# Kernel optimization log

Hardware: AMD Instinct MI355X
Metric: run time of the kernel (lower is better)

Reference implementation:

```python
import jax, jax.numpy as jnp
import numpy as np

B, T, PAST, HID = 2, 512, 4096, 4096
HQ, HKV, D = 32, 8, 128
HH_SIZE, RECENT = 512, 512
CACHE = HH_SIZE + RECENT
MAX_POS = PAST + T


def rotate_half(x):
    h = x.shape[-1] // 2
    return jnp.concatenate([-x[..., h:], x[..., :h]], axis=-1)


def setup_inputs() -> dict:
    key = jax.random.key(0)
    ks = jax.random.split(key, 9)
    hidden_states = jax.random.normal(ks[0], (B, T, HID), jnp.float32) * 0.02
    past_k = jax.random.normal(ks[1], (B, HKV, PAST, D), jnp.float32)
    past_v = jax.random.normal(ks[2], (B, HKV, PAST, D), jnp.float32)
    # accumulated heavy-hitter scores are nonnegative attention-mass sums
    hh_prev = jax.random.uniform(ks[3], (B, HKV, PAST), jnp.float32) * float(T)
    wq = jax.random.normal(ks[4], (HID, HQ * D), jnp.float32) * 0.02
    wk = jax.random.normal(ks[5], (HID, HKV * D), jnp.float32) * 0.02
    wv = jax.random.normal(ks[6], (HID, HKV * D), jnp.float32) * 0.02
    wo = jax.random.normal(ks[7], (HQ * D, HID), jnp.float32) * 0.02
    # RoPE tables [1, MAX_POS, D]
    inv_freq = 1.0 / (10000.0 ** (jnp.arange(0, D, 2, dtype=jnp.float32) / D))
    t = jnp.arange(MAX_POS, dtype=jnp.float32)
    freqs = jnp.einsum('t,f->tf', t, inv_freq)
    emb = jnp.concatenate([freqs, freqs], axis=-1)
    cos = jnp.cos(emb)[None]
    sin = jnp.sin(emb)[None]
    position_ids = jnp.broadcast_to(PAST + jnp.arange(T, dtype=jnp.int32)[None, :], (B, T))
    return {"hidden_states": hidden_states, "past_k": past_k, "past_v": past_v,
            "hh_prev": hh_prev, "wq": wq, "wk": wk, "wv": wv, "wo": wo,
            "cos": cos, "sin": sin, "position_ids": position_ids}


def reference(hidden_states, past_k, past_v, hh_prev, wq, wk, wv, wo, cos, sin, position_ids):
    b, t, _ = hidden_states.shape
    # projections -> [B, H, T, D]
    q = (hidden_states @ wq).reshape(b, t, HQ, D).transpose(0, 2, 1, 3)
    k_new = (hidden_states @ wk).reshape(b, t, HKV, D).transpose(0, 2, 1, 3)
    v_new = (hidden_states @ wv).reshape(b, t, HKV, D).transpose(0, 2, 1, 3)
    # RoPE: gather cos/sin at position_ids -> [B, 1, T, D]
    cos_g = cos[0][position_ids][:, None]
    sin_g = sin[0][position_ids][:, None]
    q = q * cos_g + rotate_half(q) * sin_g
    k_new = k_new * cos_g + rotate_half(k_new) * sin_g
    k = jnp.concatenate([past_k, k_new], axis=2)   # [B, HKV, S, D]
    v = jnp.concatenate([past_v, v_new], axis=2)
    s = k.shape[2]
    past_len = s - t
    g = HQ // HKV
    k_rep = jnp.repeat(k, g, axis=1)               # repeat_interleave over heads
    v_rep = jnp.repeat(v, g, axis=1)
    scores = jnp.einsum('bhtd,bhsd->bhts', q, k_rep) / jnp.sqrt(jnp.float32(D))
    causal = jnp.arange(s)[None, :] <= (past_len + jnp.arange(t))[:, None]  # [T, S]
    scores = jnp.where(causal[None, None], scores, jnp.finfo(scores.dtype).min)
    attn = jax.nn.softmax(scores, axis=-1)         # [B, HQ, T, S]
    ctx = jnp.einsum('bhts,bhsd->bhtd', attn, v_rep)
    out = ctx.transpose(0, 2, 1, 3).reshape(b, t, HQ * D) @ wo
    # --- H2O heavy-hitter score update ('average' GQA reduction) ---
    sc = attn.sum(axis=2)                          # [B, HQ, S]
    sc = sc.reshape(b, HKV, g, s).mean(axis=2)     # [B, HKV, S]
    hh = sc.at[:, :, :past_len].add(hh_prev)
    # --- eviction: topk heavy hitters outside recent window + recent window ---
    select = hh[:, :, : s - RECENT]
    _, top = jax.lax.top_k(select, HH_SIZE)
    top = jnp.sort(top, axis=-1)
    recent_idx = jnp.broadcast_to(jnp.arange(s - RECENT, s, dtype=top.dtype), (b, HKV, RECENT))
    keep = jnp.concatenate([top, recent_idx], axis=-1)      # [B, HKV, CACHE]
    k_kept = jnp.take_along_axis(k, keep[..., None], axis=2)
    v_kept = jnp.take_along_axis(v, keep[..., None], axis=2)
    hh_new = jnp.take_along_axis(hh, keep, axis=2)
    return out, k_kept, v_kept, hh_new
```

## Files before the change

### kernel.cpp

```cpp
#include <hip/hip_runtime.h>
#include <cstdint>
#include <cstddef>

typedef unsigned short u16;
typedef __attribute__((ext_vector_type(8))) short short8;
typedef __attribute__((ext_vector_type(4))) float floatx4;

static __device__ __forceinline__ u16 f2bf(float f){
  union { float f; uint32_t i; } u; u.f = f;
  uint32_t i = u.i;
  return (u16)((i + 0x7FFFu + ((i >> 16) & 1u)) >> 16);
}

struct __align__(8) U16x4 { u16 a,b,c,d; };

__global__ void k_convert(const float* __restrict__ src, u16* __restrict__ dst, int n4){
  int i = blockIdx.x*256 + threadIdx.x;
  if (i >= n4) return;
  float4 v = ((const float4*)src)[i];
  U16x4 o{f2bf(v.x), f2bf(v.y), f2bf(v.z), f2bf(v.w)};
  ((U16x4*)dst)[i] = o;
}

__global__ void k_copy_pastk(const float* __restrict__ pk, u16* __restrict__ kcat){
  int i = blockIdx.x*256 + threadIdx.x;
  int slice = i >> 17;
  int off   = i & 131071;
  float4 v = ((const float4*)pk)[i];
  U16x4 o{f2bf(v.x), f2bf(v.y), f2bf(v.z), f2bf(v.w)};
  ((U16x4*)(kcat + (size_t)slice*(4608*128)))[off] = o;
}

__global__ void k_transpose(const float* __restrict__ src, u16* __restrict__ dst,
                            int lds_, int ldd, size_t sstride, size_t dstride){
  src += (size_t)blockIdx.z * sstride; dst += (size_t)blockIdx.z * dstride;
  __shared__ float tile[32][33];
  int bm = blockIdx.y*32, bn = blockIdx.x*32;
  int tx = threadIdx.x & 31, ty = threadIdx.x >> 5;
  #pragma unroll
  for (int r = 0; r < 32; r += 8)
    tile[r+ty][tx] = src[(size_t)(bm + r + ty)*lds_ + bn + tx];
  __syncthreads();
  #pragma unroll
  for (int r = 0; r < 32; r += 8)
    dst[(size_t)(bn + r + ty)*ldd + bm + tx] = f2bf(tile[tx][r+ty]);
}

__global__ __launch_bounds__(256) void k_gemm_bt(
    const u16* __restrict__ A, const u16* __restrict__ Bt, float* __restrict__ C,
    int N, int Kfull, int kLen, size_t cstride)
{
  __shared__ __align__(16) u16 As[128*64];
  __shared__ __align__(16) u16 Bs[128*64];
  const int tid = threadIdx.x, lane = tid & 63, wave = tid >> 6;
  const int m0 = blockIdx.y*128, n0 = blockIdx.x*128;
  const int kOff = blockIdx.z * kLen;
  C += (size_t)blockIdx.z * cstride;
  const int wr = (wave >> 1)*64, wc = (wave & 1)*64;
  const int srow = tid >> 3, sc8 = tid & 7;
  const u16* ap = A  + (size_t)(m0 + srow)*Kfull + kOff + sc8*8;
  const u16* bp = Bt + (size_t)(n0 + srow)*Kfull + kOff + sc8*8;
  floatx4 acc[4][4] = {};
  short8 ra[4], rb[4];
  #pragma unroll
  for (int i = 0; i < 4; ++i){
    ra[i] = *(const short8*)(ap + (size_t)i*32*Kfull);
    rb[i] = *(const short8*)(bp + (size_t)i*32*Kfull);
  }
  const int nk = kLen >> 6;
  for (int kt = 0; kt < nk; ++kt){
    #pragma unroll
    for (int i = 0; i < 4; ++i){
      const int r = srow + i*32;
      const int c = sc8 ^ (r & 7);
      *(short8*)(As + r*64 + c*8) = ra[i];
      *(short8*)(Bs + r*64 + c*8) = rb[i];
    }
    __syncthreads();
    if (kt + 1 < nk){
      const size_t ko = (size_t)(kt+1)*64;
      #pragma unroll
      for (int i = 0; i < 4; ++i){
        ra[i] = *(const short8*)(ap + (size_t)i*32*Kfull + ko);
        rb[i] = *(const short8*)(bp + (size_t)i*32*Kfull + ko);
      }
    }
    #pragma unroll
    for (int ks = 0; ks < 2; ++ks){
      const int c16 = ks*4 + (lane >> 4);
      short8 af[4], bf[4];
      #pragma unroll
      for (int mi = 0; mi < 4; ++mi){
        const int r = wr + mi*16 + (lane & 15);
        af[mi] = *(const short8*)(As + r*64 + ((c16 ^ (r & 7))*8));
      }
      #pragma unroll
      for (int ni = 0; ni < 4; ++ni){
        const int r = wc + ni*16 + (lane & 15);
        bf[ni] = *(const short8*)(Bs + r*64 + ((c16 ^ (r & 7))*8));
      }
      #pragma unroll
      for (int mi = 0; mi < 4; ++mi)
        #pragma unroll
        for (int ni = 0; ni < 4; ++ni)
          acc[mi][ni] = __builtin_amdgcn_mfma_f32_16x16x32_bf16(af[mi], bf[ni], acc[mi][ni], 0,0,0);
    }
    __syncthreads();
  }
  #pragma unroll
  for (int mi = 0; mi < 4; ++mi)
    #pragma unroll
    for (int ni = 0; ni < 4; ++ni){
      const int col = n0 + wc + ni*16 + (lane & 15);
      const int row = m0 + wr + mi*16 + ((lane >> 4) << 2);
      #pragma unroll
      for (int j = 0; j < 4; ++j)
        C[(size_t)(row + j)*N + col] = acc[mi][ni][j];
    }
}

__global__ void k_add(const float* __restrict__ a, const float* __restrict__ b,
                      float* __restrict__ o, int n4){
  int i = blockIdx.x*256 + threadIdx.x;
  if (i >= n4) return;
  float4 x = ((const float4*)a)[i], y = ((const float4*)b)[i];
  float4 z; z.x=x.x+y.x; z.y=x.y+y.y; z.z=x.z+y.z; z.w=x.w+y.w;
  ((float4*)o)[i] = z;
}

__global__ void k_rope_q(const float* __restrict__ qfA, const float* __restrict__ qfB,
                         const float* __restrict__ cosb, const float* __restrict__ sinb,
                         const int* __restrict__ pid, u16* __restrict__ qbo){
  int gid = blockIdx.x*256 + threadIdx.x;
  int d = gid & 63, hh = (gid >> 6) & 31, m = gid >> 11;
  int b = m >> 9, t = m & 511;
  int p = pid[b*512 + t];
  float c = cosb[(size_t)p*128 + d], s = sinb[(size_t)p*128 + d];
  size_t ib = (size_t)m*4096 + hh*128 + d;
  float x = qfA[ib] + qfB[ib], y = qfA[ib+64] + qfB[ib+64];
  const float sc = 0.08838834764831845f;
  size_t ob = (((size_t)(b*32 + hh))*512 + t)*128 + d;
  qbo[ob]      = f2bf((x*c - y*s)*sc);
  qbo[ob + 64] = f2bf((y*c + x*s)*sc);
}

__global__ void k_rope_kv(const float* __restrict__ kvfA, const float* __restrict__ kvfB,
                          const float* __restrict__ cosb, const float* __restrict__ sinb,
                          const int* __restrict__ pid,
                          u16* __restrict__ kcat, u16* __restrict__ vtcat){
  int gid = blockIdx.x*256 + threadIdx.x;
  int d = gid & 63, kv = (gid >> 6) & 7, m = gid >> 9;
  int b = m >> 9, t = m & 511;
  int p = pid[b*512 + t];
  float c = cosb[(size_t)p*128 + d], s = sinb[(size_t)p*128 + d];
  size_t ib = (size_t)m*2048 + kv*128 + d;
  float x = kvfA[ib] + kvfB[ib], y = kvfA[ib+64] + kvfB[ib+64];
  float k0 = x*c - y*s, k1 = y*c + x*s;
  int bk = b*8 + kv;
  size_t kb = ((size_t)bk*4608 + 4096 + t)*128 + d;
  kcat[kb] = f2bf(k0); kcat[kb + 64] = f2bf(k1);
  float v0 = kvfA[ib+1024] + kvfB[ib+1024];
  float v1 = kvfA[ib+1088] + kvfB[ib+1088];
  size_t vb = (size_t)bk*(128*4608) + (size_t)d*4608 + 4096 + t;
  vtcat[vb] = f2bf(v0);
  vtcat[vb + (size_t)64*4608] = f2bf(v1);
}

__global__ __launch_bounds__(256) void k_attn_l(
    const u16* __restrict__ qb, const u16* __restrict__ kcat,
    float* __restrict__ lpart)
{
  __shared__ __align__(16) u16 kl[64*128];
  const int tid = threadIdx.x, lane = tid & 63, wave = tid >> 6;
  const int bid = blockIdx.x;
  const int slice = (bid & 7) + 8*(bid >> 10);
  const int within = (bid >> 3) & 127;
  const int b = slice >> 3, kv = slice & 7;
  const int h = kv*4 + (within >> 5);
  const int tb = (within >> 2) & 7;
  const int sc = within & 3;
  const int t0 = tb*64;
  const int ntiles = 65 + tb;
  const int st0 = sc*18;
  const int st1 = (st0 + 18 < ntiles) ? (st0 + 18) : ntiles;
  const u16* qp = qb + (((size_t)(b*32+h))*512 + t0)*128;
  const u16* kp = kcat + (size_t)slice*(4608*128);

  short8 qf[4];
  {
    const int r = wave*16 + (lane & 15);
    const u16* q0 = qp + (size_t)r*128 + ((lane>>4)*8);
    #pragma unroll
    for (int ks=0; ks<4; ++ks) qf[ks] = *(const short8*)(q0 + ks*32);
  }
  const int c16 = tid & 15, srow = tid >> 4;
  short8 rk[4];
  #pragma unroll
  for (int i=0;i<4;++i)
    rk[i] = *(const short8*)(kp + (size_t)(st0*64 + i*16 + srow)*128 + c16*8);

  float l0=0.f,l1=0.f,l2=0.f,l3=0.f;
  for (int st=st0; st<st1; ++st){
    __syncthreads();
    #pragma unroll
    for (int i=0;i<4;++i){
      const int row = i*16 + srow;
      *(short8*)(kl + row*128 + ((c16 ^ (row&7))*8)) = rk[i];
    }
    __syncthreads();
    if (st+1 < st1){
      #pragma unroll
      for (int i=0;i<4;++i)
        rk[i] = *(const short8*)(kp + (size_t)((st+1)*64 + i*16 + srow)*128 + c16*8);
    }
    floatx4 sacc[4] = {};
    #pragma unroll
    for (int ks=0; ks<4; ++ks){
      const int cc = ks*4 + (lane>>4);
      #pragma unroll
      for (int nf=0; nf<4; ++nf){
        const int r = nf*16 + (lane&15);
        short8 kf = *(const short8*)(kl + r*128 + ((cc ^ (r&7))*8));
        sacc[nf] = __builtin_amdgcn_mfma_f32_16x16x32_bf16(qf[ks], kf, sacc[nf], 0,0,0);
      }
    }
    const bool lastt = (st == ntiles-1);
    #pragma unroll
    for (int nf=0;nf<4;++nf)
      #pragma unroll
      for (int j=0;j<4;++j){
        float e = __expf(sacc[nf][j]);
        if (lastt){
          int scol = nf*16 + (lane&15);
          int tloc = wave*16 + ((lane>>4)<<2) + j;
          if (scol > tloc) e = 0.f;
        }
        if(j==0)l0+=e; else if(j==1)l1+=e; else if(j==2)l2+=e; else l3+=e;
      }
  }
  #pragma unroll
  for (int m=1; m<=8; m<<=1){
    l0 += __shfl_xor(l0,m); l1 += __shfl_xor(l1,m);
    l2 += __shfl_xor(l2,m); l3 += __shfl_xor(l3,m);
  }
  if ((lane & 15) == 0){
    float* lp = lpart + ((((size_t)(b*32+h))*8 + tb)<<8) + (sc<<6) + wave*16 + ((lane>>4)<<2);
    lp[0]=l0; lp[1]=l1; lp[2]=l2; lp[3]=l3;
  }
}

__global__ __launch_bounds__(256) void k_attn_pv(
    const u16* __restrict__ qb, const u16* __restrict__ kcat,
    const u16* __restrict__ vtcat, const float* __restrict__ lpart,
    u16* __restrict__ ctxb, float* __restrict__ part)
{
  __shared__ __align__(16) u16 kl[64*128];
  __shared__ __align__(16) u16 vl[128*64];
  __shared__ __align__(16) float plds[64*68];
  __shared__ float cw[4*64];

  const int tid=threadIdx.x, lane=tid&63, wave=tid>>6;
  const int bid=blockIdx.x;
  const int slice = (bid&7) + 8*((bid>>3)>>5);
  const int within = (bid>>3)&31;
  const int b=slice>>3, kv=slice&7;
  const int h = kv*4 + (within>>3);
  const int tb = within&7;
  const int t0 = tb*64;
  const int ntiles = 65+tb;
  const u16* qp = qb + (((size_t)(b*32+h))*512 + t0)*128;
  const u16* kp = kcat + (size_t)slice*(4608*128);
  const u16* vp = vtcat + (size_t)slice*(128*4608);
  float* pb = part + (((size_t)(b*32+h))*8 + tb)*4608;

  float rl[4];
  {
    const float* lp = lpart + ((((size_t)(b*32+h))*8 + tb)<<8);
    const int r0 = wave*16 + ((lane>>4)<<2);
    #pragma unroll
    for (int j=0;j<4;++j){
      int r = r0 + j;
      float l = lp[r] + lp[64+r] + lp[128+r] + lp[192+r];
      rl[j] = 1.f/l;
    }
  }
  short8 qf[4];
  {
    const int r = wave*16 + (lane & 15);
    const u16* q0 = qp + (size_t)r*128 + ((lane>>4)*8);
    #pragma unroll
    for (int ks=0; ks<4; ++ks) qf[ks] = *(const short8*)(q0 + ks*32);
  }
  const int c16 = tid&15, srow = tid>>4;
  const int vc = tid&7,  vrow = tid>>3;
  short8 rk[4], rv[4];
  #pragma unroll
  for (int i=0;i<4;++i){
    rk[i] = *(const short8*)(kp + (size_t)(i*16 + srow)*128 + c16*8);
    rv[i] = *(const short8*)(vp + (size_t)(i*32 + vrow)*4608 + vc*8);
  }
  floatx4 pacc[8] = {};
  const int prow = wave*16 + (lane&15);

  for (int st=0; st<ntiles; ++st){
    const int s0 = st*64;
    __syncthreads();
    if (st > 0 && tid < 64)
      pb[s0-64+tid] = cw[tid] + cw[64+tid] + cw[128+tid] + cw[192+tid];
    #pragma unroll
    for (int i=0;i<4;++i){
      const int row = i*16 + srow;
      *(short8*)(kl + row*128 + ((c16 ^ (row&7))*8)) = rk[i];
      const int vr = i*32 + vrow;
      *(short8*)(vl + vr*64 + ((vc ^ (vr&7))*8)) = rv[i];
    }
    __syncthreads();
    if (st+1 < ntiles){
      #pragma unroll
      for (int i=0;i<4;++i){
        rk[i] = *(const short8*)(kp + (size_t)((st+1)*64 + i*16 + srow)*128 + c16*8);
        rv[i] = *(const short8*)(vp + (size_t)(i*32 + vrow)*4608 + (st+1)*64 + vc*8);
      }
    }
    floatx4 sacc[4] = {};
    #pragma unroll
    for (int ks=0; ks<4; ++ks){
      const int cc = ks*4 + (lane>>4);
      #pragma unroll
      for (int nf=0; nf<4; ++nf){
        const int r = nf*16 + (lane&15);
        short8 kf = *(const short8*)(kl + r*128 + ((cc ^ (r&7))*8));
        sacc[nf] = __builtin_amdgcn_mfma_f32_16x16x32_bf16(qf[ks], kf, sacc[nf], 0,0,0);
      }
    }
    const bool lastt = (st==ntiles-1);
    float cs0=0.f, cs1=0.f, cs2=0.f, cs3=0.f;
    #pragma unroll
    for (int nf=0;nf<4;++nf){
      float cpart=0.f;
      #pragma unroll
      for (int j=0;j<4;++j){
        float e = __expf(sacc[nf][j]);
        if (lastt){
          int scol = nf*16 + (lane&15);
          int tloc = wave*16 + ((lane>>4)<<2) + j;
          if (scol > tloc) e = 0.f;
        }
        float p = e * rl[j];
        plds[(wave*16 + ((lane>>4)<<2) + j)*68 + nf*16 + (lane&15)] = p;
        cpart += p;
      }
      if(nf==0)cs0=cpart; else if(nf==1)cs1=cpart; else if(nf==2)cs2=cpart; else cs3=cpart;
    }
    cs0 += __shfl_xor(cs0,16); cs0 += __shfl_xor(cs0,32);
    cs1 += __shfl_xor(cs1,16); cs1 += __shfl_xor(cs1,32);
    cs2 += __shfl_xor(cs2,16); cs2 += __shfl_xor(cs2,32);
    cs3 += __shfl_xor(cs3,16); cs3 += __shfl_xor(cs3,32);
    {
      const int nfsel = lane >> 4;
      float v = (nfsel==0)?cs0:(nfsel==1)?cs1:(nfsel==2)?cs2:cs3;
      cw[wave*64 + nfsel*16 + (lane & 15)] = v;
    }
    short8 pa[2];
    #pragma unroll
    for (int k2 = 0; k2 < 2; ++k2){
      const int sbase = k2*32 + ((lane>>4)*8);
      const float* pp = plds + prow*68 + sbase;
      float4 x = *(const float4*)pp;
      float4 y = *(const float4*)(pp + 4);
      short8 t8;
      t8[0]=(short)f2bf(x.x); t8[1]=(short)f2bf(x.y); t8[2]=(short)f2bf(x.z); t8[3]=(short)f2bf(x.w);
      t8[4]=(short)f2bf(y.x); t8[5]=(short)f2bf(y.y); t8[6]=(short)f2bf(y.z); t8[7]=(short)f2bf(y.w);
      pa[k2] = t8;
    }
    #pragma unroll
    for (int nf = 0; nf < 8; ++nf){
      const int rv2 = nf*16 + (lane & 15);
      #pragma unroll
      for (int k2 = 0; k2 < 2; ++k2){
        const int c = ((k2*4 + (lane>>4)) ^ (rv2 & 7));
        short8 vf = *(const short8*)(vl + rv2*64 + c*8);
        pacc[nf] = __builtin_amdgcn_mfma_f32_16x16x32_bf16(pa[k2], vf, pacc[nf], 0,0,0);
      }
    }
  }
  __syncthreads();
  if (tid < 64)
    pb[(ntiles-1)*64 + tid] = cw[tid] + cw[64+tid] + cw[128+tid] + cw[192+tid];
  #pragma unroll
  for (int nf = 0; nf < 8; ++nf)
    #pragma unroll
    for (int j = 0; j < 4; ++j){
      const int trow = t0 + wave*16 + ((lane>>4)<<2) + j;
      const int col  = h*128 + nf*16 + (lane & 15);
      ctxb[(size_t)(b*512 + trow)*4096 + col] = f2bf(pacc[nf][j]);
    }
}

__global__ void k_hh_reduce(const float* __restrict__ part, const float* __restrict__ hhprev,
                            float* __restrict__ hh){
  int gid = blockIdx.x*256 + threadIdx.x;
  if (gid >= 73728) return;
  int s = gid % 4608; int bk = gid / 4608; int b = bk >> 3, kv = bk & 7;
  float acc = 0.f;
  #pragma unroll
  for (int h4 = 0; h4 < 4; ++h4){
    const float* pp = part + (((size_t)(b*32 + kv*4 + h4))*8)*4608 + s;
    #pragma unroll
    for (int tbb = 0; tbb < 8; ++tbb)
      if (s < 4160 + tbb*64) acc += pp[(size_t)tbb*4608];
  }
  acc *= 0.25f;
  if (s < 4096) acc += hhprev[(size_t)bk*4096 + s];
  hh[gid] = acc;
}

__global__ __launch_bounds__(256) void k_topk(const float* __restrict__ hh, int* __restrict__ keep,
                                              float* __restrict__ hh_new){
  __shared__ uint64_t keys[4096];
  __shared__ int sidx[512];
  const int bk = blockIdx.x, tid = threadIdx.x;
  const float* hp = hh + (size_t)bk*4608;
  for (int i = tid; i < 4096; i += 256){
    uint32_t vb = __float_as_uint(hp[i]);
    keys[i] = ((uint64_t)(0xFFFFFFFFu - vb) << 12) | (uint32_t)i;
  }
  __syncthreads();
  for (int k = 2; k <= 4096; k <<= 1){
    for (int j = k >> 1; j > 0; j >>= 1){
      for (int i = tid; i < 4096; i += 256){
        int ixj = i ^ j;
        if (ixj > i){
          uint64_t a = keys[i], c = keys[ixj];
          bool up = ((i & k) == 0);
          if ((a > c) == up){ keys[i] = c; keys[ixj] = a; }
        }
      }
      __syncthreads();
    }
  }
  for (int i = tid; i < 512; i += 256) sidx[i] = (int)(keys[i] & 0xFFF);
  __syncthreads();
  for (int k = 2; k <= 512; k <<= 1){
    for (int j = k >> 1; j > 0; j >>= 1){
      for (int i = tid; i < 512; i += 256){
        int ixj = i ^ j;
        if (ixj > i){
          int a = sidx[i], c = sidx[ixj];
          bool up = ((i & k) == 0);
          if ((a > c) == up){ sidx[i] = c; sidx[ixj] = a; }
        }
      }
      __syncthreads();
    }
  }
  for (int i = tid; i < 512; i += 256){
    int id = sidx[i];
    keep[bk*1024 + i] = id;
    hh_new[(size_t)bk*1024 + i] = hp[id];
    keep[bk*1024 + 512 + i] = 4096 + i;
    hh_new[(size_t)bk*1024 + 512 + i] = hp[4096 + i];
  }
}

__global__ void k_gather(const float* __restrict__ pastk, const float* __restrict__ pastv,
                         const float* __restrict__ kvfA, const float* __restrict__ kvfB,
                         const float* __restrict__ cosb, const float* __restrict__ sinb,
                         const int* __restrict__ pid, const int* __restrict__ keep,
                         float* __restrict__ outk, float* __restrict__ outv){
  int r = blockIdx.x*2 + (threadIdx.x >> 7);
  int d = threadIdx.x & 127;
  int bk = r >> 10, i = r & 1023;
  int idx = keep[bk*1024 + i];
  float kval, vval;
  if (idx < 4096){
    kval = pastk[((size_t)bk*4096 + idx)*128 + d];
    vval = pastv[((size_t)bk*4096 + idx)*128 + d];
  } else {
    int t = idx - 4096; int b = bk >> 3, kv = bk & 7;
    size_t base = ((size_t)(b*512 + t))*2048 + kv*128;
    int dp = (d < 64) ? d + 64 : d - 64;
    float x  = kvfA[base + d]  + kvfB[base + d];
    float xp = kvfA[base + dp] + kvfB[base + dp];
    int p = pid[b*512 + t];
    float c = cosb[(size_t)p*128 + d], s = sinb[(size_t)p*128 + d];
    kval = x*c + xp*((d < 64) ? -s : s);
    vval = kvfA[base + 1024 + d] + kvfB[base + 1024 + d];
  }
  outk[(size_t)r*128 + d] = kval;
  outv[(size_t)r*128 + d] = vval;
}

extern "C" void kernel_launch(void* const* d_in, const int* in_sizes, int n_in,
                              void* d_out, int out_size, void* d_ws, size_t ws_size,
                              hipStream_t stream){
  const float* hs     = (const float*)d_in[0];
  const float* pastk  = (const float*)d_in[1];
  const float* pastv  = (const float*)d_in[2];
  const float* hhprev = (const float*)d_in[3];
  const float* wq     = (const float*)d_in[4];
  const float* wk     = (const float*)d_in[5];
  const float* wv     = (const float*)d_in[6];
  const float* wo     = (const float*)d_in[7];
  const float* cosb   = (const float*)d_in[8];
  const float* sinb   = (const float*)d_in[9];
  const int*   pid    = (const int*)d_in[10];
  float* out = (float*)d_out;
  char* ws = (char*)d_ws;

  u16*   hsb  = (u16*)(ws + 0);
  u16*   wqt  = (u16*)(ws + 8388608);
  u16*   wkvt = (u16*)(ws + 41943040);
  float* qfA  = (float*)(ws + 58720256);
  float* qfB  = (float*)(ws + 75497472);
  float* kvfA = (float*)(ws + 92274688);
  float* kvfB = (float*)(ws + 100663296);
  u16*   qb   = (u16*)(ws + 109051904);
  u16*   kcat = (u16*)(ws + 117440512);
  u16*   vtc  = (u16*)(ws + 136314880);
  u16*   ctxb = (u16*)(ws + 155189248);
  float* part = (float*)(ws + 163577856);
  float* lprt = (float*)(ws + 173015040);
  float* hhb  = (float*)(ws + 173539328);
  int*   keep = (int*)(ws + 173834240);

  (void)in_sizes; (void)n_in; (void)out_size; (void)ws_size;

  k_convert<<<4096,256,0,stream>>>(hs, hsb, 1048576);
  k_transpose<<<dim3(128,128,1),256,0,stream>>>(wq, wqt, 4096, 4096, 0, 0);
  k_transpose<<<dim3(32,128,1),256,0,stream>>>(wk, wkvt, 1024, 4096, 0, 0);
  k_transpose<<<dim3(32,128,1),256,0,stream>>>(wv, wkvt + (size_t)1024*4096, 1024, 4096, 0, 0);
  k_transpose<<<dim3(4,128,16),256,0,stream>>>(pastv, vtc, 128, 4608,
                                               (size_t)4096*128, (size_t)128*4608);
  k_copy_pastk<<<8192,256,0,stream>>>(pastk, kcat);

  k_gemm_bt<<<dim3(32,8,2),256,0,stream>>>(hsb, wqt, qfA, 4096, 4096, 2048, (size_t)1024*4096);
  k_gemm_bt<<<dim3(16,8,2),256,0,stream>>>(hsb, wkvt, kvfA, 2048, 4096, 2048, (size_t)1024*2048);
  k_transpose<<<dim3(128,128,1),256,0,stream>>>(wo, wqt, 4096, 4096, 0, 0);

  k_rope_q<<<8192,256,0,stream>>>(qfA, qfB, cosb, sinb, pid, qb);
  k_rope_kv<<<2048,256,0,stream>>>(kvfA, kvfB, cosb, sinb, pid, kcat, vtc);

  k_attn_l<<<2048,256,0,stream>>>(qb, kcat, lprt);
  k_attn_pv<<<512,256,0,stream>>>(qb, kcat, vtc, lprt, ctxb, part);

  k_gemm_bt<<<dim3(32,8,2),256,0,stream>>>(ctxb, wqt, qfA, 4096, 4096, 2048, (size_t)1024*4096);
  k_add<<<4096,256,0,stream>>>(qfA, qfB, out, 1048576);

  k_hh_reduce<<<288,256,0,stream>>>(part, hhprev, hhb);
  k_topk<<<16,256,0,stream>>>(hhb, keep, out + 8388608);
  k_gather<<<8192,256,0,stream>>>(pastk, pastv, kvfA, kvfB, cosb, sinb, pid, keep,
                                  out + 4194304, out + 6291456);
}
```

Baseline: 789.3 us.

## Split attention PV over key halves, radix-select top-k, direct-to-LDS GEMM loads

Doubles the attention PV grid by splitting each query tile's key range into two halves that write fp32 partial contexts, then adds a combine kernel that sums them and converts to bf16. The GEMM now loads tiles with global_load_lds straight into swizzled LDS instead of staging them through registers, which drops the software prefetch. Top-k replaces the full 4096-element bitonic sort and index sort with a radix select plus prefix-sum compaction, so indices come out already in ascending order. The PV kernel also uses packed bf16 convert instructions. The costs are an extra kernel and fp32 traffic for the partial contexts, and less load/compute overlap in the GEMM.

Result: faster. 725.6 us (-8.1%).

```diff
diff --git a/kernel.cpp b/kernel.cpp
--- a/kernel.cpp
+++ b/kernel.cpp
@@ -12,7 +12,20 @@
   return (u16)((i + 0x7FFFu + ((i >> 16) & 1u)) >> 16);
 }
 
+static __device__ __forceinline__ void gload_lds16(const u16* g, u16* l){
+  __builtin_amdgcn_global_load_lds(
+      (const __attribute__((address_space(1))) uint32_t*)g,
+      (__attribute__((address_space(3))) uint32_t*)l, 16, 0, 0);
+}
+
+static __device__ __forceinline__ uint32_t cvtpk(float lo, float hi){
+  uint32_t r;
+  asm("v_cvt_pk_bf16_f32 %0, %1, %2" : "=v"(r) : "v"(lo), "v"(hi));
+  return r;
+}
+
 struct __align__(8) U16x4 { u16 a,b,c,d; };
+union PU { short8 s; uint32_t u[4]; };
 
 __global__ void k_convert(const float* __restrict__ src, u16* __restrict__ dst, int n4){
   int i = blockIdx.x*256 + threadIdx.x;
@@ -58,33 +71,22 @@
   C += (size_t)blockIdx.z * cstride;
   const int wr = (wave >> 1)*64, wc = (wave & 1)*64;
   const int srow = tid >> 3, sc8 = tid & 7;
-  const u16* ap = A  + (size_t)(m0 + srow)*Kfull + kOff + sc8*8;
-  const u16* bp = Bt + (size_t)(n0 + srow)*Kfull + kOff + sc8*8;
+  const int csw = (sc8 ^ (srow & 7)) * 8;
+  const u16* ap = A  + (size_t)(m0 + srow)*Kfull + kOff + csw;
+  const u16* bp = Bt + (size_t)(n0 + srow)*Kfull + kOff + csw;
+  u16* la = As + wave*512;
+  u16* lb = Bs + wave*512;
   floatx4 acc[4][4] = {};
-  short8 ra[4], rb[4];
-  #pragma unroll
-  for (int i = 0; i < 4; ++i){
-    ra[i] = *(const short8*)(ap + (size_t)i*32*Kfull);
-    rb[i] = *(const short8*)(bp + (size_t)i*32*Kfull);
-  }
   const int nk = kLen >> 6;
   for (int kt = 0; kt < nk; ++kt){
+    if (kt) __syncthreads();
+    const size_t ko = (size_t)kt*64;
     #pragma unroll
     for (int i = 0; i < 4; ++i){
-      const int r = srow + i*32;
-      const int c = sc8 ^ (r & 7);
-      *(short8*)(As + r*64 + c*8) = ra[i];
-      *(short8*)(Bs + r*64 + c*8) = rb[i];
-    }
-    __syncthreads();
-    if (kt + 1 < nk){
-      const size_t ko = (size_t)(kt+1)*64;
-      #pragma unroll
-      for (int i = 0; i < 4; ++i){
-        ra[i] = *(const short8*)(ap + (size_t)i*32*Kfull + ko);
-        rb[i] = *(const short8*)(bp + (size_t)i*32*Kfull + ko);
-      }
-    }
+      gload_lds16(ap + (size_t)i*32*Kfull + ko, la + i*2048);
+      gload_lds16(bp + (size_t)i*32*Kfull + ko, lb + i*2048);
+    }
+    __syncthreads();
     #pragma unroll
     for (int ks = 0; ks < 2; ++ks){
       const int c16 = ks*4 + (lane >> 4);
@@ -105,7 +107,6 @@
         for (int ni = 0; ni < 4; ++ni)
           acc[mi][ni] = __builtin_amdgcn_mfma_f32_16x16x32_bf16(af[mi], bf[ni], acc[mi][ni], 0,0,0);
     }
-    __syncthreads();
   }
   #pragma unroll
   for (int mi = 0; mi < 4; ++mi)
@@ -126,6 +127,15 @@
   float4 x = ((const float4*)a)[i], y = ((const float4*)b)[i];
   float4 z; z.x=x.x+y.x; z.y=x.y+y.y; z.z=x.z+y.z; z.w=x.w+y.w;
   ((float4*)o)[i] = z;
+}
+
+__global__ void k_ctx_combine(const float* __restrict__ a, const float* __restrict__ b,
+                              u16* __restrict__ o, int n4){
+  int i = blockIdx.x*256 + threadIdx.x;
+  if (i >= n4) return;
+  float4 x = ((const float4*)a)[i], y = ((const float4*)b)[i];
+  U16x4 r{f2bf(x.x+y.x), f2bf(x.y+y.y), f2bf(x.z+y.z), f2bf(x.w+y.w)};
+  ((U16x4*)o)[i] = r;
 }
 
 __global__ void k_rope_q(const float* __restrict__ qfA, const float* __restrict__ qfB,
@@ -252,7 +262,7 @@
 __global__ __launch_bounds__(256) void k_attn_pv(
     const u16* __restrict__ qb, const u16* __restrict__ kcat,
     const u16* __restrict__ vtcat, const float* __restrict__ lpart,
-    u16* __restrict__ ctxb, float* __restrict__ part)
+    float* __restrict__ ctxp, float* __restrict__ part)
 {
   __shared__ __align__(16) u16 kl[64*128];
   __shared__ __align__(16) u16 vl[128*64];
@@ -261,17 +271,21 @@
 
   const int tid=threadIdx.x, lane=tid&63, wave=tid>>6;
   const int bid=blockIdx.x;
-  const int slice = (bid&7) + 8*((bid>>3)>>5);
-  const int within = (bid>>3)&31;
+  const int slice = (bid&7) + 8*((bid>>3)>>6);
+  const int within = (bid>>3)&63;
   const int b=slice>>3, kv=slice&7;
-  const int h = kv*4 + (within>>3);
-  const int tb = within&7;
+  const int h  = kv*4 + (within>>4);
+  const int tb = (within>>1)&7;
+  const int hlf = within&1;
   const int t0 = tb*64;
   const int ntiles = 65+tb;
+  const int st0 = hlf ? 33 : 0;
+  const int st1 = hlf ? ntiles : 33;
   const u16* qp = qb + (((size_t)(b*32+h))*512 + t0)*128;
   const u16* kp = kcat + (size_t)slice*(4608*128);
   const u16* vp = vtcat + (size_t)slice*(128*4608);
   float* pb = part + (((size_t)(b*32+h))*8 + tb)*4608;
+  float* cp = ctxp + (size_t)hlf*4194304;
 
   float rl[4];
   {
@@ -296,16 +310,16 @@
   short8 rk[4], rv[4];
   #pragma unroll
   for (int i=0;i<4;++i){
-    rk[i] = *(const short8*)(kp + (size_t)(i*16 + srow)*128 + c16*8);
-    rv[i] = *(const short8*)(vp + (size_t)(i*32 + vrow)*4608 + vc*8);
+    rk[i] = *(const short8*)(kp + (size_t)(st0*64 + i*16 + srow)*128 + c16*8);
+    rv[i] = *(const short8*)(vp + (size_t)(i*32 + vrow)*4608 + st0*64 + vc*8);
   }
   floatx4 pacc[8] = {};
   const int prow = wave*16 + (lane&15);
 
-  for (int st=0; st<ntiles; ++st){
+  for (int st=st0; st<st1; ++st){
     const int s0 = st*64;
     __syncthreads();
-    if (st > 0 && tid < 64)
+    if (st > st0 && tid < 64)
       pb[s0-64+tid] = cw[tid] + cw[64+tid] + cw[128+tid] + cw[192+tid];
     #pragma unroll
     for (int i=0;i<4;++i){
@@ -315,7 +329,7 @@
       *(short8*)(vl + vr*64 + ((vc ^ (vr&7))*8)) = rv[i];
     }
     __syncthreads();
-    if (st+1 < ntiles){
+    if (st+1 < st1){
       #pragma unroll
       for (int i=0;i<4;++i){
         rk[i] = *(const short8*)(kp + (size_t)((st+1)*64 + i*16 + srow)*128 + c16*8);
@@ -364,14 +378,15 @@
     short8 pa[2];
     #pragma unroll
     for (int k2 = 0; k2 < 2; ++k2){
-      const int sbase = k2*32 + ((lane>>4)*8);
-      const float* pp = plds + prow*68 + sbase;
+      const float* pp = plds + prow*68 + k2*32 + ((lane>>4)*8);
       float4 x = *(const float4*)pp;
       float4 y = *(const float4*)(pp + 4);
-      short8 t8;
-      t8[0]=(short)f2bf(x.x); t8[1]=(short)f2bf(x.y); t8[2]=(short)f2bf(x.z); t8[3]=(short)f2bf(x.w);
-      t8[4]=(short)f2bf(y.x); t8[5]=(short)f2bf(y.y); t8[6]=(short)f2bf(y.z); t8[7]=(short)f2bf(y.w);
-      pa[k2] = t8;
+      PU t;
+      t.u[0] = cvtpk(x.x, x.y);
+      t.u[1] = cvtpk(x.z, x.w);
+      t.u[2] = cvtpk(y.x, y.y);
+      t.u[3] = cvtpk(y.z, y.w);
+      pa[k2] = t.s;
     }
     #pragma unroll
     for (int nf = 0; nf < 8; ++nf){
@@ -386,14 +401,14 @@
   }
   __syncthreads();
   if (tid < 64)
-    pb[(ntiles-1)*64 + tid] = cw[tid] + cw[64+tid] + cw[128+tid] + cw[192+tid];
+    pb[(st1-1)*64 + tid] = cw[tid] + cw[64+tid] + cw[128+tid] + cw[192+tid];
   #pragma unroll
   for (int nf = 0; nf < 8; ++nf)
     #pragma unroll
     for (int j = 0; j < 4; ++j){
       const int trow = t0 + wave*16 + ((lane>>4)<<2) + j;
       const int col  = h*128 + nf*16 + (lane & 15);
-      ctxb[(size_t)(b*512 + trow)*4096 + col] = f2bf(pacc[nf][j]);
+      cp[(size_t)(b*512 + trow)*4096 + col] = pacc[nf][j];
     }
 }
 
@@ -418,46 +433,58 @@
 __global__ __launch_bounds__(256) void k_topk(const float* __restrict__ hh, int* __restrict__ keep,
                                               float* __restrict__ hh_new){
   __shared__ uint64_t keys[4096];
-  __shared__ int sidx[512];
+  __shared__ int hist[256];
+  __shared__ int tsum[256];
+  __shared__ uint64_t sprefix;
+  __shared__ int srank;
   const int bk = blockIdx.x, tid = threadIdx.x;
   const float* hp = hh + (size_t)bk*4608;
   for (int i = tid; i < 4096; i += 256){
     uint32_t vb = __float_as_uint(hp[i]);
     keys[i] = ((uint64_t)(0xFFFFFFFFu - vb) << 12) | (uint32_t)i;
   }
+  if (tid == 0){ sprefix = 0; srank = 512; }
   __syncthreads();
-  for (int k = 2; k <= 4096; k <<= 1){
-    for (int j = k >> 1; j > 0; j >>= 1){
-      for (int i = tid; i < 4096; i += 256){
-        int ixj = i ^ j;
-        if (ixj > i){
-          uint64_t a = keys[i], c = keys[ixj];
-          bool up = ((i & k) == 0);
-          if ((a > c) == up){ keys[i] = c; keys[ixj] = a; }
-        }
-      }
-      __syncthreads();
-    }
-  }
-  for (int i = tid; i < 512; i += 256) sidx[i] = (int)(keys[i] & 0xFFF);
+  for (int shift = 40; shift >= 0; shift -= 8){
+    hist[tid] = 0;
+    __syncthreads();
+    const uint64_t pref = sprefix;
+    const uint64_t hm = ~((1ull << (shift+8)) - 1ull);
+    for (int i = tid; i < 4096; i += 256){
+      uint64_t k = keys[i];
+      if ((k & hm) == pref) atomicAdd(&hist[(int)((k >> shift) & 255)], 1);
+    }
+    __syncthreads();
+    if (tid == 0){
+      int r = srank, b = 0;
+      for (;;){ int c = hist[b]; if (r <= c) break; r -= c; ++b; }
+      srank = r; sprefix = pref | ((uint64_t)b << shift);
+    }
+    __syncthreads();
+  }
+  const uint64_t kstar = sprefix;
+  const int base = tid*16;
+  int cnt = 0;
+  #pragma unroll
+  for (int j = 0; j < 16; ++j) cnt += (keys[base+j] <= kstar) ? 1 : 0;
+  tsum[tid] = cnt;
   __syncthreads();
-  for (int k = 2; k <= 512; k <<= 1){
-    for (int j = k >> 1; j > 0; j >>= 1){
-      for (int i = tid; i < 512; i += 256){
-        int ixj = i ^ j;
-        if (ixj > i){
-          int a = sidx[i], c = sidx[ixj];
-          bool up = ((i & k) == 0);
-          if ((a > c) == up){ sidx[i] = c; sidx[ixj] = a; }
-        }
-      }
-      __syncthreads();
+  for (int off = 1; off < 256; off <<= 1){
+    int v = (tid >= off) ? tsum[tid-off] : 0;
+    __syncthreads();
+    tsum[tid] += v;
+    __syncthreads();
+  }
+  int pos = tsum[tid] - cnt;
+  for (int j = 0; j < 16; ++j){
+    uint64_t k = keys[base+j];
+    if (k <= kstar){
+      keep[bk*1024 + pos] = base + j;
+      hh_new[(size_t)bk*1024 + pos] = __uint_as_float(0xFFFFFFFFu - (uint32_t)(k >> 12));
+      ++pos;
     }
   }
   for (int i = tid; i < 512; i += 256){
-    int id = sidx[i];
-    keep[bk*1024 + i] = id;
-    hh_new[(size_t)bk*1024 + i] = hp[id];
     keep[bk*1024 + 512 + i] = 4096 + i;
     hh_new[(size_t)bk*1024 + 512 + i] = hp[4096 + i];
   }
@@ -542,7 +569,8 @@
   k_rope_kv<<<2048,256,0,stream>>>(kvfA, kvfB, cosb, sinb, pid, kcat, vtc);
 
   k_attn_l<<<2048,256,0,stream>>>(qb, kcat, lprt);
-  k_attn_pv<<<512,256,0,stream>>>(qb, kcat, vtc, lprt, ctxb, part);
+  k_attn_pv<<<1024,256,0,stream>>>(qb, kcat, vtc, lprt, qfA, part);
+  k_ctx_combine<<<4096,256,0,stream>>>(qfA, qfB, ctxb, 1048576);
 
   k_gemm_bt<<<dim3(32,8,2),256,0,stream>>>(ctxb, wqt, qfA, 4096, 4096, 2048, (size_t)1024*4096);
   k_add<<<4096,256,0,stream>>>(qfA, qfB, out, 1048576);
```
